# Optimization experiments

Measured on AMD Instinct MI355X. Metric: run time of the kernel, lower is better.

Reference implementation:

```python
import jax, jax.numpy as jnp
import numpy as np

MIN_SCALE = 1e-3
TEMPERATURE = 1.5


def setup_inputs() -> dict:
    key = jax.random.key(0)
    ks = jax.random.split(key, 9)
    B, S, D, R, C = 1024, 64, 512, 16, 1000
    s = 1.0 / np.sqrt(D)  # scale weights for numerical sanity
    return {
        "features": jax.random.normal(ks[0], (B, D), jnp.float32),
        "W_cov": jax.random.normal(ks[1], (D * R, D), jnp.float32) * s,
        "b_cov": jnp.zeros((D * R,), jnp.float32),
        "W_diag": jax.random.normal(ks[2], (D, D), jnp.float32) * s,
        "b_diag": jnp.zeros((D,), jnp.float32),
        "W_cls": jax.random.normal(ks[3], (C, D), jnp.float32) * s,
        "b_cls": jnp.zeros((C,), jnp.float32),
        "noise_diag": jax.random.normal(ks[4], (B, S, D), jnp.float32),
        "noise_lr": jax.random.normal(ks[5], (B, S, R), jnp.float32),
    }


def reference(features, W_cov, b_cov, W_diag, b_diag, W_cls, b_cls, noise_diag, noise_lr):
    B, D = features.shape
    R = noise_lr.shape[-1]
    # Linear(D -> D*R), reshape to (B, D, R) (row-major, matches torch .reshape)
    low_rank_cov = (features @ W_cov.T + b_cov).reshape(B, D, R)
    # diagonal std: softplus(Linear(D->D)) + min_scale
    diagonal_std = jax.nn.softplus(features @ W_diag.T + b_diag) + MIN_SCALE
    # samples: low-rank part + diagonal part, both (B, S, D)
    samples = (
        jnp.einsum("bdr,bsr->bsd", low_rank_cov, noise_lr)
        + diagonal_std[:, None, :] * noise_diag
    )
    pre_logits = features[:, None, :] + samples  # (B, S, D)
    logits = pre_logits @ W_cls.T + b_cls  # (B, S, C)
    return logits / TEMPERATURE
```

## Files before the change

### kernel.cpp

```cpp
#include <hip/hip_runtime.h>
#include <math.h>

typedef __attribute__((ext_vector_type(8))) short bf16x8;
typedef __attribute__((ext_vector_type(4))) float f32x4;
typedef __attribute__((ext_vector_type(4))) unsigned short u16x4;

__device__ inline unsigned short f2bf(float f) {
    union { float f; unsigned u; } v; v.f = f;
    unsigned r = v.u + 0x7FFFu + ((v.u >> 16) & 1u);
    return (unsigned short)(r >> 16);
}
__device__ inline float bf2f(unsigned short h) {
    union { unsigned u; float f; } v; v.u = ((unsigned)h) << 16;
    return v.f;
}

__device__ inline void load_lds16(const void* g, void* l) {
    __builtin_amdgcn_global_load_lds(
        (const __attribute__((address_space(1))) unsigned int*)g,
        (__attribute__((address_space(3))) unsigned int*)l,
        16, 0, 0);
}

__global__ __launch_bounds__(256) void convert_all(
    const float* __restrict__ sA, unsigned short* __restrict__ dA, long nA,
    const float* __restrict__ sB, unsigned short* __restrict__ dB, long nB,
    const float* __restrict__ sC, unsigned short* __restrict__ dC, long nC,
    const float* __restrict__ sD, unsigned short* __restrict__ dD, long nDs, long nDd)
{
    long i = ((long)blockIdx.x * 256 + threadIdx.x) * 4;
    const float* s; unsigned short* d; long nsrc;
    if (i < nA)              { s = sA + i; d = dA + i; nsrc = nA - i; }
    else if ((i -= nA) < nB) { s = sB + i; d = dB + i; nsrc = nB - i; }
    else if ((i -= nB) < nC) { s = sC + i; d = dC + i; nsrc = nC - i; }
    else if ((i -= nC) < nDd){ s = sD + i; d = dD + i; nsrc = nDs - i; }
    else return;
    float4 v = make_float4(0.f, 0.f, 0.f, 0.f);
    if (nsrc >= 4) v = *(const float4*)s;
    u16x4 o;
    o[0] = f2bf(v.x); o[1] = f2bf(v.y); o[2] = f2bf(v.z); o[3] = f2bf(v.w);
    *(u16x4*)d = o;
}

template <int MODE, bool SWZ>
__global__ __launch_bounds__(256) void gemm_bf16(
    const unsigned short* __restrict__ A, const unsigned short* __restrict__ Bm,
    const float* __restrict__ bias0, const float* __restrict__ bias1,
    void* __restrict__ out0v, void* __restrict__ out1v,
    int M, int Npad, int Nreal, int K, int nsplit)
{
    __shared__ __align__(16) unsigned short As[128 * 64];
    __shared__ __align__(16) unsigned short Bs[128 * 64];

    const int tid  = threadIdx.x;
    const int nblk = Npad >> 7;
    int mt, nt;
    if constexpr (SWZ) {
        const int per = (M >> 7) >> 3;
        const int x = blockIdx.x & 7;
        const int j = blockIdx.x >> 3;
        const int jm = j / nblk;
        mt = x * per + jm;
        nt = j - jm * nblk;
    } else {
        mt = blockIdx.x / nblk;
        nt = blockIdx.x - mt * nblk;
    }
    const int m0 = mt << 7;
    const int n0 = nt << 7;

    const int lane = tid & 63;
    const int wid  = tid >> 6;
    const int wm   = (wid & 1) << 6;
    const int wn   = (wid >> 1) << 6;
    const int quad = lane >> 4;
    const int l15  = lane & 15;
    const int l7   = l15 & 7;

    const int lrow = lane >> 3;
    const int lcol = ((lane & 7) ^ lrow) << 3;

    const unsigned short* Ab = A  + (size_t)(m0 + wid * 32 + lrow) * K + lcol;
    const unsigned short* Bb = Bm + (size_t)(n0 + wid * 32 + lrow) * K + lcol;
    unsigned short* AsW = &As[(wid * 32) * 64];
    unsigned short* BsW = &Bs[(wid * 32) * 64];

    f32x4 acc[4][4];
    #pragma unroll
    for (int i = 0; i < 4; ++i)
        #pragma unroll
        for (int j = 0; j < 4; ++j)
            acc[i][j] = f32x4{0.f, 0.f, 0.f, 0.f};

    for (int kt = 0; kt < K; kt += 64) {
        __syncthreads();
        #pragma unroll
        for (int i = 0; i < 4; ++i) {
            load_lds16(Ab + (size_t)(i * 8) * K + kt, AsW + i * 8 * 64);
            load_lds16(Bb + (size_t)(i * 8) * K + kt, BsW + i * 8 * 64);
        }
        __syncthreads();

        #pragma unroll
        for (int kk = 0; kk < 64; kk += 32) {
            const int kq = kk >> 3;
            bf16x8 af[4], bfv[4];
            #pragma unroll
            for (int mi = 0; mi < 4; ++mi)
                af[mi] = *(const bf16x8*)&As[(wm + mi * 16 + l15) * 64
                                             + (((kq + quad) ^ l7) << 3)];
            #pragma unroll
            for (int ni = 0; ni < 4; ++ni)
                bfv[ni] = *(const bf16x8*)&Bs[(wn + ni * 16 + l15) * 64
                                              + (((kq + quad) ^ l7) << 3)];
            #pragma unroll
            for (int mi = 0; mi < 4; ++mi)
                #pragma unroll
                for (int ni = 0; ni < 4; ++ni)
                    acc[mi][ni] = __builtin_amdgcn_mfma_f32_16x16x32_bf16(
                        af[mi], bfv[ni], acc[mi][ni], 0, 0, 0);
        }
    }

    #pragma unroll
    for (int ni = 0; ni < 4; ++ni) {
        const int n = n0 + wn + ni * 16 + l15;
        if constexpr (MODE == 2) {
            const bool nok = n < Nreal;
            const float bv = nok ? bias0[n] : 0.f;
            float* o = (float*)out0v;
            #pragma unroll
            for (int mi = 0; mi < 4; ++mi) {
                const int mb = m0 + wm + mi * 16 + quad * 4;
                #pragma unroll
                for (int r = 0; r < 4; ++r) {
                    float v = (acc[mi][ni][r] + bv) * (1.0f / 1.5f);
                    if (nok) o[(size_t)(mb + r) * Nreal + n] = v;
                }
            }
        } else {
            if (n0 < nsplit) {
                const float bv = bias0[n];
                unsigned short* o = (unsigned short*)out0v;
                #pragma unroll
                for (int mi = 0; mi < 4; ++mi) {
                    const int mb = m0 + wm + mi * 16 + quad * 4;
                    #pragma unroll
                    for (int r = 0; r < 4; ++r)
                        o[(size_t)(mb + r) * nsplit + n] = f2bf(acc[mi][ni][r] + bv);
                }
            } else {
                const int n1 = n - nsplit;
                const int ld1 = Npad - nsplit;
                const float bv = bias1[n1];
                float* o = (float*)out1v;
                #pragma unroll
                for (int mi = 0; mi < 4; ++mi) {
                    const int mb = m0 + wm + mi * 16 + quad * 4;
                    #pragma unroll
                    for (int r = 0; r < 4; ++r) {
                        float v = acc[mi][ni][r] + bv;
                        float sp = (v > 20.f) ? v : log1pf(expf(v));
                        o[(size_t)(mb + r) * ld1 + n1] = sp + 1e-3f;
                    }
                }
            }
        }
    }
}

__global__ __launch_bounds__(256) void sample_kernel(
    const float* __restrict__ features, const unsigned short* __restrict__ lr_cov,
    const float* __restrict__ diag, const float* __restrict__ nz_lr,
    const float* __restrict__ nz_diag, unsigned short* __restrict__ pre,
    int S, int D)
{
    const int tid = threadIdx.x;
    const int bl  = tid >> 7;
    const int b   = blockIdx.x * 2 + bl;
    const int t   = tid & 127;
    const int d0  = t << 2;

    __shared__ float snz[2][64 * 16];
    {
        const float* zsrc = nz_lr + (size_t)(blockIdx.x * 2) * S * 16;
        for (int j = tid; j < 2 * S * 16; j += 256)
            ((float*)snz)[j] = zsrc[j];
    }

    float4 f  = *(const float4*)(features + (size_t)b * D + d0);
    float4 dg = *(const float4*)(diag + (size_t)b * D + d0);
    float L[4][16];
    const unsigned short* lp = lr_cov + (size_t)b * D * 16 + (size_t)d0 * 16;
    #pragma unroll
    for (int j = 0; j < 4; ++j) {
        bf16x8 a = *(const bf16x8*)(lp + j * 16);
        bf16x8 c = *(const bf16x8*)(lp + j * 16 + 8);
        #pragma unroll
        for (int r = 0; r < 8; ++r) {
            L[j][r]     = bf2f((unsigned short)a[r]);
            L[j][8 + r] = bf2f((unsigned short)c[r]);
        }
    }
    __syncthreads();

    const float* ndp = nz_diag + (size_t)b * S * D + d0;
    unsigned short* pp = pre + (size_t)b * S * D + d0;
    for (int s = 0; s < S; ++s) {
        float4 nd = *(const float4*)(ndp + (size_t)s * D);
        float o0 = f.x + dg.x * nd.x;
        float o1 = f.y + dg.y * nd.y;
        float o2 = f.z + dg.z * nd.z;
        float o3 = f.w + dg.w * nd.w;
        const float* z = &snz[bl][s * 16];
        #pragma unroll
        for (int r = 0; r < 16; ++r) {
            float zv = z[r];
            o0 += L[0][r] * zv; o1 += L[1][r] * zv;
            o2 += L[2][r] * zv; o3 += L[3][r] * zv;
        }
        u16x4 o;
        o[0] = f2bf(o0); o[1] = f2bf(o1); o[2] = f2bf(o2); o[3] = f2bf(o3);
        *(u16x4*)(pp + (size_t)s * D) = o;
    }
}

extern "C" void kernel_launch(void* const* d_in, const int* in_sizes, int n_in,
                              void* d_out, int out_size, void* d_ws, size_t ws_size,
                              hipStream_t stream)
{
    const float* features = (const float*)d_in[0];
    const float* W_cov    = (const float*)d_in[1];
    const float* b_cov    = (const float*)d_in[2];
    const float* W_diag   = (const float*)d_in[3];
    const float* b_diag   = (const float*)d_in[4];
    const float* W_cls    = (const float*)d_in[5];
    const float* b_cls    = (const float*)d_in[6];
    const float* nz_diag  = (const float*)d_in[7];
    const float* nz_lr    = (const float*)d_in[8];

    const int D    = in_sizes[4];
    const int DR   = in_sizes[2];
    const int B    = in_sizes[0] / D;
    const int S    = in_sizes[7] / (B * D);
    const int C    = in_sizes[6];
    const int M    = B * S;
    const int Cpad = (C + 127) & ~127;
    const int Ncat = DR + D;

    char* ws = (char*)d_ws;
    unsigned short* lrcov = (unsigned short*)ws;
    float*          diag  = (float*)(ws + (size_t)B * DR * 2);
    unsigned short* wclsb = (unsigned short*)((char*)diag + (size_t)B * D * 4);
    char* X = (char*)wclsb + (size_t)Cpad * D * 2;
    unsigned short* featb = (unsigned short*)X;
    unsigned short* wcatb = featb + (size_t)B * D;
    unsigned short* pre   = (unsigned short*)X;

    {
        long n1 = (long)DR * D;
        long n2 = (long)D * D;
        long n3 = (long)B * D;
        long n4s = (long)C * D, n4d = (long)Cpad * D;
        long total = n1 + n2 + n3 + n4d;
        convert_all<<<dim3((unsigned)(total / 1024)), 256, 0, stream>>>(
            W_cov, wcatb, n1,
            W_diag, wcatb + n1, n2,
            features, featb, n3,
            W_cls, wclsb, n4s, n4d);
    }

    gemm_bf16<3, false><<<dim3((B / 128) * (Ncat / 128)), 256, 0, stream>>>(
        featb, wcatb, b_cov, b_diag, lrcov, diag, B, Ncat, Ncat, D, DR);

    sample_kernel<<<dim3(B / 2), 256, 0, stream>>>(
        features, lrcov, diag, nz_lr, nz_diag, pre, S, D);

    gemm_bf16<2, true><<<dim3((M / 128) * (Cpad / 128)), 256, 0, stream>>>(
        pre, wclsb, b_cls, nullptr, d_out, nullptr, M, Cpad, C, D, DR);
}
```

Before: 562.5 us.

## Transpose MFMA output for vectorized epilogue stores and split sampling per batch

Swaps the MFMA operand order so each lane holds four consecutive N columns, which lets the GEMM epilogues load bias as float4 and write 16-byte fp32 or 8-byte bf16 vectors instead of scalar strided stores. The sample kernel now assigns one batch row per block, with the two half-blocks splitting the S samples and each thread processing two samples per iteration. The goal is better-coalesced output writes and more parallelism and ILP in the memory-bound sampling step. The MODE 2 path skips a whole 4-column group when its first column is past Nreal, which depends on C being a multiple of 4.

```diff
diff --git a/kernel.cpp b/kernel.cpp
--- a/kernel.cpp
+++ b/kernel.cpp
@@ -118,51 +118,64 @@
                 #pragma unroll
                 for (int ni = 0; ni < 4; ++ni)
                     acc[mi][ni] = __builtin_amdgcn_mfma_f32_16x16x32_bf16(
-                        af[mi], bfv[ni], acc[mi][ni], 0, 0, 0);
-        }
-    }
-
-    #pragma unroll
-    for (int ni = 0; ni < 4; ++ni) {
-        const int n = n0 + wn + ni * 16 + l15;
-        if constexpr (MODE == 2) {
-            const bool nok = n < Nreal;
-            const float bv = nok ? bias0[n] : 0.f;
-            float* o = (float*)out0v;
+                        bfv[ni], af[mi], acc[mi][ni], 0, 0, 0);
+        }
+    }
+
+    if constexpr (MODE == 2) {
+        float* o = (float*)out0v;
+        #pragma unroll
+        for (int ni = 0; ni < 4; ++ni) {
+            const int nb = n0 + wn + ni * 16 + (quad << 2);
+            if (nb >= Nreal) continue;
+            const float4 bv = *(const float4*)&bias0[nb];
             #pragma unroll
             for (int mi = 0; mi < 4; ++mi) {
-                const int mb = m0 + wm + mi * 16 + quad * 4;
+                const int m = m0 + wm + mi * 16 + l15;
+                f32x4 v;
+                v[0] = (acc[mi][ni][0] + bv.x) * (1.0f / 1.5f);
+                v[1] = (acc[mi][ni][1] + bv.y) * (1.0f / 1.5f);
+                v[2] = (acc[mi][ni][2] + bv.z) * (1.0f / 1.5f);
+                v[3] = (acc[mi][ni][3] + bv.w) * (1.0f / 1.5f);
+                *(f32x4*)&o[(size_t)m * Nreal + nb] = v;
+            }
+        }
+    } else {
+        if (n0 < nsplit) {
+            unsigned short* o = (unsigned short*)out0v;
+            #pragma unroll
+            for (int ni = 0; ni < 4; ++ni) {
+                const int nb = n0 + wn + ni * 16 + (quad << 2);
+                const float4 bv = *(const float4*)&bias0[nb];
                 #pragma unroll
-                for (int r = 0; r < 4; ++r) {
-                    float v = (acc[mi][ni][r] + bv) * (1.0f / 1.5f);
-                    if (nok) o[(size_t)(mb + r) * Nreal + n] = v;
+                for (int mi = 0; mi < 4; ++mi) {
+                    const int m = m0 + wm + mi * 16 + l15;
+                    u16x4 ov;
+                    ov[0] = f2bf(acc[mi][ni][0] + bv.x);
+                    ov[1] = f2bf(acc[mi][ni][1] + bv.y);
+                    ov[2] = f2bf(acc[mi][ni][2] + bv.z);
+                    ov[3] = f2bf(acc[mi][ni][3] + bv.w);
+                    *(u16x4*)&o[(size_t)m * nsplit + nb] = ov;
                 }
             }
         } else {
-            if (n0 < nsplit) {
-                const float bv = bias0[n];
-                unsigned short* o = (unsigned short*)out0v;
+            float* o = (float*)out1v;
+            const int ld1 = Npad - nsplit;
+            #pragma unroll
+            for (int ni = 0; ni < 4; ++ni) {
+                const int nb = n0 + wn + ni * 16 + (quad << 2) - nsplit;
+                const float4 bv = *(const float4*)&bias1[nb];
                 #pragma unroll
                 for (int mi = 0; mi < 4; ++mi) {
-                    const int mb = m0 + wm + mi * 16 + quad * 4;
-                    #pragma unroll
-                    for (int r = 0; r < 4; ++r)
-                        o[(size_t)(mb + r) * nsplit + n] = f2bf(acc[mi][ni][r] + bv);
-                }
-            } else {
-                const int n1 = n - nsplit;
-                const int ld1 = Npad - nsplit;
-                const float bv = bias1[n1];
-                float* o = (float*)out1v;
-                #pragma unroll
-                for (int mi = 0; mi < 4; ++mi) {
-                    const int mb = m0 + wm + mi * 16 + quad * 4;
+                    const int m = m0 + wm + mi * 16 + l15;
+                    f32x4 v;
                     #pragma unroll
                     for (int r = 0; r < 4; ++r) {
-                        float v = acc[mi][ni][r] + bv;
-                        float sp = (v > 20.f) ? v : log1pf(expf(v));
-                        o[(size_t)(mb + r) * ld1 + n1] = sp + 1e-3f;
+                        float x = acc[mi][ni][r] + ((const float*)&bv)[r];
+                        float sp = (x > 20.f) ? x : log1pf(expf(x));
+                        v[r] = sp + 1e-3f;
                     }
+                    *(f32x4*)&o[(size_t)m * ld1 + nb] = v;
                 }
             }
         }
@@ -176,17 +189,13 @@
     int S, int D)
 {
     const int tid = threadIdx.x;
-    const int bl  = tid >> 7;
-    const int b   = blockIdx.x * 2 + bl;
+    const int b   = blockIdx.x;
+    const int sh  = tid >> 7;
     const int t   = tid & 127;
     const int d0  = t << 2;
 
-    __shared__ float snz[2][64 * 16];
-    {
-        const float* zsrc = nz_lr + (size_t)(blockIdx.x * 2) * S * 16;
-        for (int j = tid; j < 2 * S * 16; j += 256)
-            ((float*)snz)[j] = zsrc[j];
-    }
+    __shared__ __align__(16) float snz[64 * 16];
+    ((float4*)snz)[tid] = ((const float4*)(nz_lr + (size_t)b * S * 16))[tid];
 
     float4 f  = *(const float4*)(features + (size_t)b * D + d0);
     float4 dg = *(const float4*)(diag + (size_t)b * D + d0);
@@ -204,24 +213,32 @@
     }
     __syncthreads();
 
-    const float* ndp = nz_diag + (size_t)b * S * D + d0;
-    unsigned short* pp = pre + (size_t)b * S * D + d0;
-    for (int s = 0; s < S; ++s) {
-        float4 nd = *(const float4*)(ndp + (size_t)s * D);
-        float o0 = f.x + dg.x * nd.x;
-        float o1 = f.y + dg.y * nd.y;
-        float o2 = f.z + dg.z * nd.z;
-        float o3 = f.w + dg.w * nd.w;
-        const float* z = &snz[bl][s * 16];
+    const int s0 = sh * (S >> 1);
+    const float* ndp = nz_diag + (size_t)b * S * D + (size_t)s0 * D + d0;
+    unsigned short* pp = pre + (size_t)b * S * D + (size_t)s0 * D + d0;
+    const int SH = S >> 1;
+    for (int s = 0; s < SH; s += 2) {
+        float4 nd0 = *(const float4*)(ndp + (size_t)s * D);
+        float4 nd1 = *(const float4*)(ndp + (size_t)(s + 1) * D);
+        float a0 = f.x + dg.x * nd0.x, a1 = f.y + dg.y * nd0.y;
+        float a2 = f.z + dg.z * nd0.z, a3 = f.w + dg.w * nd0.w;
+        float b0 = f.x + dg.x * nd1.x, b1 = f.y + dg.y * nd1.y;
+        float b2 = f.z + dg.z * nd1.z, b3 = f.w + dg.w * nd1.w;
+        const float* z0 = &snz[(s0 + s) * 16];
+        const float* z1 = &snz[(s0 + s + 1) * 16];
         #pragma unroll
         for (int r = 0; r < 16; ++r) {
-            float zv = z[r];
-            o0 += L[0][r] * zv; o1 += L[1][r] * zv;
-            o2 += L[2][r] * zv; o3 += L[3][r] * zv;
-        }
-        u16x4 o;
-        o[0] = f2bf(o0); o[1] = f2bf(o1); o[2] = f2bf(o2); o[3] = f2bf(o3);
-        *(u16x4*)(pp + (size_t)s * D) = o;
+            float zv0 = z0[r], zv1 = z1[r];
+            a0 += L[0][r] * zv0; a1 += L[1][r] * zv0;
+            a2 += L[2][r] * zv0; a3 += L[3][r] * zv0;
+            b0 += L[0][r] * zv1; b1 += L[1][r] * zv1;
+            b2 += L[2][r] * zv1; b3 += L[3][r] * zv1;
+        }
+        u16x4 o0, o1;
+        o0[0] = f2bf(a0); o0[1] = f2bf(a1); o0[2] = f2bf(a2); o0[3] = f2bf(a3);
+        o1[0] = f2bf(b0); o1[1] = f2bf(b1); o1[2] = f2bf(b2); o1[3] = f2bf(b3);
+        *(u16x4*)(pp + (size_t)s * D) = o0;
+        *(u16x4*)(pp + (size_t)(s + 1) * D) = o1;
     }
 }
 
@@ -273,7 +290,7 @@
     gemm_bf16<3, false><<<dim3((B / 128) * (Ncat / 128)), 256, 0, stream>>>(
         featb, wcatb, b_cov, b_diag, lrcov, diag, B, Ncat, Ncat, D, DR);
 
-    sample_kernel<<<dim3(B / 2), 256, 0, stream>>>(
+    sample_kernel<<<dim3(B), 256, 0, stream>>>(
         features, lrcov, diag, nz_lr, nz_diag, pre, S, D);
 
     gemm_bf16<2, true><<<dim3((M / 128) * (Cpad / 128)), 256, 0, stream>>>(
```

New measurement: 547.1 us. 1.03x faster.
